# Kernel optimization log

Measured on AMD Instinct MI355X. Metric: run time of the kernel, lower is better.

The kernel has to match this reference:

```python
import jax, jax.numpy as jnp
import numpy as np

N = 100_000      # nodes
DEG = 16         # avg in-degree (fixed per node for setup)
E = N * DEG      # edges
IN = 256         # in_feats
H = 4            # num_heads
D = 64           # out_feats per head
NEG_SLOPE = 0.2


def setup_inputs() -> dict:
    key = jax.random.key(0)
    k1, k2, k3, k4, k5 = jax.random.split(key, 5)
    # dst-major CSR with uniform degree DEG per destination node
    row_ptr = jnp.arange(N + 1, dtype=jnp.int32) * DEG          # [N+1]
    col_ind = jax.random.randint(k1, (E,), 0, N, dtype=jnp.int32)  # source ids per edge
    feat = jax.random.normal(k2, (N, IN), dtype=jnp.float32)
    # fc.weight (xavier-ish scale), torch Linear: y = x @ W.T
    W = jax.random.normal(k3, (H * D, IN), dtype=jnp.float32) * (1.0 / np.sqrt(IN))
    attn_l = jax.random.normal(k4, (1, H, D), dtype=jnp.float32) * 0.1
    attn_r = jax.random.normal(k5, (1, H, D), dtype=jnp.float32) * 0.1
    return {"row_ptr": row_ptr, "col_ind": col_ind, "feat": feat,
            "W": W, "attn_l": attn_l, "attn_r": attn_r}


def reference(row_ptr, col_ind, feat, W, attn_l, attn_r):
    n_nodes = feat.shape[0]
    n_edges = col_ind.shape[0]
    # feat_src = feat_dst = fc(feat).view(-1, H, D)
    feat_src = (feat @ W.T).reshape(n_nodes, H, D)
    el = jnp.sum(feat_src * attn_l, axis=-1)   # [N, H]
    er = jnp.sum(feat_src * attn_r, axis=-1)   # [N, H]
    # per-edge dst id from CSR row_ptr; src = col_ind
    dst = (jnp.searchsorted(row_ptr, jnp.arange(n_edges, dtype=row_ptr.dtype),
                            side='right') - 1).astype(jnp.int32)
    src = col_ind
    # e = u_add_v(g, er, el) -> er[src] + el[dst], then LeakyReLU
    e = er[src] + el[dst]                      # [E, H]
    e = jnp.where(e > 0, e, NEG_SLOPE * e)
    # CSR edge-softmax: normalize over incoming edges of each dst row
    m = jax.ops.segment_max(e, dst, num_segments=n_nodes)    # [N, H]
    ex = jnp.exp(e - m[dst])
    s = jax.ops.segment_sum(ex, dst, num_segments=n_nodes)   # [N, H]
    a = ex / s[dst]                                          # [E, H]
    # multi-head SpMM: out[n,h] = sum_{e: dst=n} a[e,h] * feat_src[src[e],h]
    outs = []
    for h in range(H):  # small fixed head loop to avoid [E,H,D] intermediate
        msg = a[:, h, None] * feat_src[src, h]               # [E, D]
        outs.append(jax.ops.segment_sum(msg, dst, num_segments=n_nodes))
    return jnp.stack(outs, axis=1)                           # [N, H, D]
```

## Files before the change

kernel.cpp:

```cpp
#include <hip/hip_runtime.h>
#include <math.h>


#define HEADS 4
#define KIN 256
#define NOUT 256
#define NEG_SLOPE 0.2f

typedef __attribute__((ext_vector_type(4))) short short4v;
typedef __attribute__((ext_vector_type(8))) short short8v;
typedef __attribute__((ext_vector_type(4))) float floatx4;

static __device__ __forceinline__ unsigned short f2bf(float x) {
  unsigned u = __float_as_uint(x);
  u += 0x7FFFu + ((u >> 16) & 1u);
  return (unsigned short)(u >> 16);
}
static __device__ __forceinline__ float bf2f(unsigned short b) {
  return __uint_as_float(((unsigned)b) << 16);
}

__global__ __launch_bounds__(256) void k_cast_w(const float* __restrict__ W,
                                                unsigned short* __restrict__ Wbf) {
  const int i = blockIdx.x * 256 + threadIdx.x;
  float4 f = ((const float4*)W)[i];
  ushort4 o;
  o.x = f2bf(f.x); o.y = f2bf(f.y); o.z = f2bf(f.z); o.w = f2bf(f.w);
  ((ushort4*)Wbf)[i] = o;
}

__global__ __launch_bounds__(256, 2) void k_gemm_mfma(
    const float* __restrict__ feat, const unsigned short* __restrict__ Wbf,
    const float* __restrict__ attn_l, const float* __restrict__ attn_r,
    unsigned short* __restrict__ fs_bf, float* __restrict__ el,
    float* __restrict__ er, int n_nodes) {
  __shared__ unsigned short Alds[2][64 * 64];

  const int tid = threadIdx.x;
  const int lane = tid & 63;
  const int w = tid >> 6;
  const int m0 = blockIdx.x * 64;
  const int q = lane >> 4;
  const int l15 = lane & 15;

  floatx4 acc[4][4];
#pragma unroll
  for (int mt = 0; mt < 4; ++mt)
#pragma unroll
    for (int nt = 0; nt < 4; ++nt)
#pragma unroll
      for (int r = 0; r < 4; ++r) acc[mt][nt][r] = 0.0f;

  const int ar = tid >> 2;
  const int aj = tid & 3;
  const int r7 = ar & 7;
  int agr = m0 + ar;
  if (agr >= n_nodes) agr = n_nodes - 1;
  const float* __restrict__ abase = feat + (size_t)agr * KIN + aj * 16;
  unsigned short* const aw0 = &Alds[0][ar * 64 + ((2 * aj + 0) ^ r7) * 8];
  unsigned short* const aw1 = &Alds[0][ar * 64 + ((2 * aj + 1) ^ r7) * 8];
  const int bufoff = 64 * 64;

  float4 rg[2][4];

#pragma unroll
  for (int i = 0; i < 4; ++i) rg[0][i] = *(const float4*)(abase + i * 4);

#pragma unroll
  for (int kc = 0; kc < 4; ++kc) {
    const int b = kc & 1;
    {
      const float4* R = rg[b];
      short8v g0, g1;
      g0[0] = (short)f2bf(R[0].x); g0[1] = (short)f2bf(R[0].y);
      g0[2] = (short)f2bf(R[0].z); g0[3] = (short)f2bf(R[0].w);
      g0[4] = (short)f2bf(R[1].x); g0[5] = (short)f2bf(R[1].y);
      g0[6] = (short)f2bf(R[1].z); g0[7] = (short)f2bf(R[1].w);
      g1[0] = (short)f2bf(R[2].x); g1[1] = (short)f2bf(R[2].y);
      g1[2] = (short)f2bf(R[2].z); g1[3] = (short)f2bf(R[2].w);
      g1[4] = (short)f2bf(R[3].x); g1[5] = (short)f2bf(R[3].y);
      g1[6] = (short)f2bf(R[3].z); g1[7] = (short)f2bf(R[3].w);
      *(short8v*)(aw0 + b * bufoff) = g0;
      *(short8v*)(aw1 + b * bufoff) = g1;
    }
    if (kc < 3) {
      const float* p = abase + (kc + 1) * 64;
#pragma unroll
      for (int i = 0; i < 4; ++i) rg[(kc + 1) & 1][i] = *(const float4*)(p + i * 4);
    }
    __syncthreads();

    short8v bfr[2][4];
#pragma unroll
    for (int ks = 0; ks < 2; ++ks)
#pragma unroll
      for (int nt = 0; nt < 4; ++nt)
        bfr[ks][nt] = *(const short8v*)(Wbf + (size_t)(w * 64 + nt * 16 + l15) * KIN +
                                        kc * 64 + ks * 32 + q * 8);

#pragma unroll
    for (int ks = 0; ks < 2; ++ks) {
      short8v af[4];
#pragma unroll
      for (int mt = 0; mt < 4; ++mt) {
        const int slot = (ks * 4 + q) ^ (l15 & 7);
        af[mt] = *(const short8v*)(&Alds[b][(mt * 16 + l15) * 64 + slot * 8]);
      }
#pragma unroll
      for (int mt = 0; mt < 4; ++mt)
#pragma unroll
        for (int nt = 0; nt < 4; ++nt)
          acc[mt][nt] = __builtin_amdgcn_mfma_f32_16x16x32_bf16(
              af[mt], bfr[ks][nt], acc[mt][nt], 0, 0, 0);
    }
  }

  float alv[4], arv[4];
#pragma unroll
  for (int nt = 0; nt < 4; ++nt) {
    alv[nt] = attn_l[w * 64 + nt * 16 + l15];
    arv[nt] = attn_r[w * 64 + nt * 16 + l15];
  }
#pragma unroll
  for (int mt = 0; mt < 4; ++mt) {
#pragma unroll
    for (int r = 0; r < 4; ++r) {
      const int m = m0 + mt * 16 + q * 4 + r;
      const bool mvalid = (m < n_nodes);
      float pl = 0.f, pr = 0.f;
#pragma unroll
      for (int nt = 0; nt < 4; ++nt) {
        const float v = acc[mt][nt][r];
        pl = fmaf(v, alv[nt], pl);
        pr = fmaf(v, arv[nt], pr);
        if (mvalid)
          fs_bf[(size_t)m * NOUT + w * 64 + nt * 16 + l15] = f2bf(v);
      }
#pragma unroll
      for (int off = 1; off < 16; off <<= 1) {
        pl += __shfl_xor(pl, off, 64);
        pr += __shfl_xor(pr, off, 64);
      }
      if (l15 == 0 && mvalid) {
        el[m * HEADS + w] = pl;
        er[m * HEADS + w] = pr;
      }
    }
  }
}

__global__ __launch_bounds__(256, 4) void k_aggregate(
    const int* __restrict__ row_ptr, const int* __restrict__ col_ind,
    const float* __restrict__ el, const float* __restrict__ er,
    const unsigned short* __restrict__ fs_bf, float* __restrict__ out,
    int n_nodes) {
  const int gid = blockIdx.x * blockDim.x + threadIdx.x;
  const int node = gid >> 6;
  const int lane = threadIdx.x & 63;
  if (node >= n_nodes) return;

  const int h = lane >> 4;
  const int j = lane & 15;
  const int rs = row_ptr[node];
  const int deg = row_ptr[node + 1] - rs;

  const bool valid = (j < deg);
  const int src = valid ? col_ind[rs + j] : 0;

  float e = valid ? (er[src * HEADS + h] + el[node * HEADS + h]) : -INFINITY;
  e = (e > 0.f) ? e : NEG_SLOPE * e;

  float mx = e;
#pragma unroll
  for (int off = 1; off < 16; off <<= 1) mx = fmaxf(mx, __shfl_xor(mx, off, 64));
  float ex = valid ? __expf(e - mx) : 0.f;
  float s = ex;
#pragma unroll
  for (int off = 1; off < 16; off <<= 1) s += __shfl_xor(s, off, 64);
  const float a = ex / s;

  const int half = lane >> 5;
  const int li = lane & 31;
  const int hd = li >> 3;

  int sj[8];
#pragma unroll
  for (int p = 0; p < 8; ++p) sj[p] = __shfl(src, 2 * p + half, 64);

  uint4 u[8];
#pragma unroll
  for (int p = 0; p < 8; ++p)
    u[p] = ((const uint4*)(fs_bf + (size_t)sj[p] * NOUT))[li];

  float wgt[8];
#pragma unroll
  for (int p = 0; p < 8; ++p)
    wgt[p] = __shfl(a, hd * 16 + 2 * p + half, 64);

  float acc[8];
#pragma unroll
  for (int k = 0; k < 8; ++k) acc[k] = 0.f;
#pragma unroll
  for (int p = 0; p < 8; ++p) {
    const uint4 v = u[p];
    const float w0 = wgt[p];
    acc[0] = fmaf(w0, __uint_as_float(v.x << 16), acc[0]);
    acc[1] = fmaf(w0, __uint_as_float(v.x & 0xFFFF0000u), acc[1]);
    acc[2] = fmaf(w0, __uint_as_float(v.y << 16), acc[2]);
    acc[3] = fmaf(w0, __uint_as_float(v.y & 0xFFFF0000u), acc[3]);
    acc[4] = fmaf(w0, __uint_as_float(v.z << 16), acc[4]);
    acc[5] = fmaf(w0, __uint_as_float(v.z & 0xFFFF0000u), acc[5]);
    acc[6] = fmaf(w0, __uint_as_float(v.w << 16), acc[6]);
    acc[7] = fmaf(w0, __uint_as_float(v.w & 0xFFFF0000u), acc[7]);
  }

#pragma unroll
  for (int k = 0; k < 8; ++k) acc[k] += __shfl_xor(acc[k], 32, 64);

  float4 o;
  o.x = half ? acc[4] : acc[0];
  o.y = half ? acc[5] : acc[1];
  o.z = half ? acc[6] : acc[2];
  o.w = half ? acc[7] : acc[3];
  *(float4*)(out + (size_t)node * NOUT + li * 8 + half * 4) = o;
}

extern "C" void kernel_launch(void* const* d_in, const int* in_sizes, int n_in,
                              void* d_out, int out_size, void* d_ws, size_t ws_size,
                              hipStream_t stream) {
  const int* row_ptr = (const int*)d_in[0];
  const int* col_ind = (const int*)d_in[1];
  const float* feat = (const float*)d_in[2];
  const float* W = (const float*)d_in[3];
  const float* attn_l = (const float*)d_in[4];
  const float* attn_r = (const float*)d_in[5];
  float* out = (float*)d_out;
  const int n_nodes = in_sizes[0] - 1;

  char* ws = (char*)d_ws;
  unsigned short* Wbf = (unsigned short*)ws;
  unsigned short* fs_bf = (unsigned short*)(ws + 128 * 1024);
  size_t fs_bytes = (size_t)n_nodes * NOUT * sizeof(unsigned short);
  float* el = (float*)(ws + 128 * 1024 + fs_bytes);
  float* er = el + (size_t)n_nodes * HEADS;

  k_cast_w<<<64, 256, 0, stream>>>(W, Wbf);
  k_gemm_mfma<<<(n_nodes + 63) / 64, 256, 0, stream>>>(
      feat, Wbf, attn_l, attn_r, fs_bf, el, er, n_nodes);
  k_aggregate<<<(n_nodes + 3) / 4, 256, 0, stream>>>(
      row_ptr, col_ind, el, er, fs_bf, out, n_nodes);
}
```

Measured before the change: 349.0 us.

## Store projected features head-major and split aggregation per head

Measured after the change: 380.5 us. 9.0% more time.

```diff
diff --git a/kernel.cpp b/kernel.cpp
--- a/kernel.cpp
+++ b/kernel.cpp
@@ -32,8 +32,8 @@
 __global__ __launch_bounds__(256, 2) void k_gemm_mfma(
     const float* __restrict__ feat, const unsigned short* __restrict__ Wbf,
     const float* __restrict__ attn_l, const float* __restrict__ attn_r,
-    unsigned short* __restrict__ fs_bf, float* __restrict__ el,
-    float* __restrict__ er, int n_nodes) {
+    unsigned short* __restrict__ fs_h, float* __restrict__ el_h,
+    float* __restrict__ er_h, int n_nodes) {
   __shared__ unsigned short Alds[2][64 * 64];
 
   const int tid = threadIdx.x;
@@ -134,7 +134,7 @@
         pl = fmaf(v, alv[nt], pl);
         pr = fmaf(v, arv[nt], pr);
         if (mvalid)
-          fs_bf[(size_t)m * NOUT + w * 64 + nt * 16 + l15] = f2bf(v);
+          fs_h[((size_t)w * n_nodes + m) * 64 + nt * 16 + l15] = f2bf(v);
       }
 #pragma unroll
       for (int off = 1; off < 16; off <<= 1) {
@@ -142,8 +142,8 @@
         pr += __shfl_xor(pr, off, 64);
       }
       if (l15 == 0 && mvalid) {
-        el[m * HEADS + w] = pl;
-        er[m * HEADS + w] = pr;
+        el_h[(size_t)w * n_nodes + m] = pl;
+        er_h[(size_t)w * n_nodes + m] = pr;
       }
     }
   }
@@ -151,23 +151,26 @@
 
 __global__ __launch_bounds__(256, 4) void k_aggregate(
     const int* __restrict__ row_ptr, const int* __restrict__ col_ind,
-    const float* __restrict__ el, const float* __restrict__ er,
-    const unsigned short* __restrict__ fs_bf, float* __restrict__ out,
+    const float* __restrict__ el_h, const float* __restrict__ er_h,
+    const unsigned short* __restrict__ fs_h, float* __restrict__ out,
     int n_nodes) {
-  const int gid = blockIdx.x * blockDim.x + threadIdx.x;
-  const int node = gid >> 6;
+  const int bid = blockIdx.x;
   const int lane = threadIdx.x & 63;
+  const int w = threadIdx.x >> 6;
+  const int x = bid & 7;
+  const int h = x >> 1;
+  const int idx = (bid >> 3) * 2 + (x & 1);
+  const int node = idx * 4 + w;
   if (node >= n_nodes) return;
 
-  const int h = lane >> 4;
   const int j = lane & 15;
   const int rs = row_ptr[node];
   const int deg = row_ptr[node + 1] - rs;
-
   const bool valid = (j < deg);
   const int src = valid ? col_ind[rs + j] : 0;
 
-  float e = valid ? (er[src * HEADS + h] + el[node * HEADS + h]) : -INFINITY;
+  const size_t hN = (size_t)h * n_nodes;
+  float e = valid ? (er_h[hN + src] + el_h[hN + node]) : -INFINITY;
   e = (e > 0.f) ? e : NEG_SLOPE * e;
 
   float mx = e;
@@ -179,50 +182,45 @@
   for (int off = 1; off < 16; off <<= 1) s += __shfl_xor(s, off, 64);
   const float a = ex / s;
 
-  const int half = lane >> 5;
-  const int li = lane & 31;
-  const int hd = li >> 3;
-
-  int sj[8];
-#pragma unroll
-  for (int p = 0; p < 8; ++p) sj[p] = __shfl(src, 2 * p + half, 64);
-
-  uint4 u[8];
-#pragma unroll
-  for (int p = 0; p < 8; ++p)
-    u[p] = ((const uint4*)(fs_bf + (size_t)sj[p] * NOUT))[li];
-
-  float wgt[8];
-#pragma unroll
-  for (int p = 0; p < 8; ++p)
-    wgt[p] = __shfl(a, hd * 16 + 2 * p + half, 64);
+  const int e8 = lane >> 3;
+  const int c = lane & 7;
+  const int s0 = __shfl(src, e8, 64);
+  const int s1 = __shfl(src, 8 + e8, 64);
+  const float w0 = __shfl(a, e8, 64);
+  const float w1 = __shfl(a, 8 + e8, 64);
+  const uint4 u0 = ((const uint4*)(fs_h + (hN + (size_t)s0) * 64))[c];
+  const uint4 u1 = ((const uint4*)(fs_h + (hN + (size_t)s1) * 64))[c];
 
   float acc[8];
 #pragma unroll
   for (int k = 0; k < 8; ++k) acc[k] = 0.f;
-#pragma unroll
-  for (int p = 0; p < 8; ++p) {
-    const uint4 v = u[p];
-    const float w0 = wgt[p];
-    acc[0] = fmaf(w0, __uint_as_float(v.x << 16), acc[0]);
-    acc[1] = fmaf(w0, __uint_as_float(v.x & 0xFFFF0000u), acc[1]);
-    acc[2] = fmaf(w0, __uint_as_float(v.y << 16), acc[2]);
-    acc[3] = fmaf(w0, __uint_as_float(v.y & 0xFFFF0000u), acc[3]);
-    acc[4] = fmaf(w0, __uint_as_float(v.z << 16), acc[4]);
-    acc[5] = fmaf(w0, __uint_as_float(v.z & 0xFFFF0000u), acc[5]);
-    acc[6] = fmaf(w0, __uint_as_float(v.w << 16), acc[6]);
-    acc[7] = fmaf(w0, __uint_as_float(v.w & 0xFFFF0000u), acc[7]);
-  }
-
-#pragma unroll
-  for (int k = 0; k < 8; ++k) acc[k] += __shfl_xor(acc[k], 32, 64);
-
-  float4 o;
-  o.x = half ? acc[4] : acc[0];
-  o.y = half ? acc[5] : acc[1];
-  o.z = half ? acc[6] : acc[2];
-  o.w = half ? acc[7] : acc[3];
-  *(float4*)(out + (size_t)node * NOUT + li * 8 + half * 4) = o;
+  acc[0] = fmaf(w0, __uint_as_float(u0.x << 16), acc[0]);
+  acc[1] = fmaf(w0, __uint_as_float(u0.x & 0xFFFF0000u), acc[1]);
+  acc[2] = fmaf(w0, __uint_as_float(u0.y << 16), acc[2]);
+  acc[3] = fmaf(w0, __uint_as_float(u0.y & 0xFFFF0000u), acc[3]);
+  acc[4] = fmaf(w0, __uint_as_float(u0.z << 16), acc[4]);
+  acc[5] = fmaf(w0, __uint_as_float(u0.z & 0xFFFF0000u), acc[5]);
+  acc[6] = fmaf(w0, __uint_as_float(u0.w << 16), acc[6]);
+  acc[7] = fmaf(w0, __uint_as_float(u0.w & 0xFFFF0000u), acc[7]);
+  acc[0] = fmaf(w1, __uint_as_float(u1.x << 16), acc[0]);
+  acc[1] = fmaf(w1, __uint_as_float(u1.x & 0xFFFF0000u), acc[1]);
+  acc[2] = fmaf(w1, __uint_as_float(u1.y << 16), acc[2]);
+  acc[3] = fmaf(w1, __uint_as_float(u1.y & 0xFFFF0000u), acc[3]);
+  acc[4] = fmaf(w1, __uint_as_float(u1.z << 16), acc[4]);
+  acc[5] = fmaf(w1, __uint_as_float(u1.z & 0xFFFF0000u), acc[5]);
+  acc[6] = fmaf(w1, __uint_as_float(u1.w << 16), acc[6]);
+  acc[7] = fmaf(w1, __uint_as_float(u1.w & 0xFFFF0000u), acc[7]);
+
+#pragma unroll
+  for (int off = 8; off < 64; off <<= 1)
+#pragma unroll
+    for (int k = 0; k < 8; ++k) acc[k] += __shfl_xor(acc[k], off, 64);
+
+  if (lane < 8) {
+    float* op = out + ((size_t)node * HEADS + h) * 64 + lane * 8;
+    *(float4*)op = make_float4(acc[0], acc[1], acc[2], acc[3]);
+    *(float4*)(op + 4) = make_float4(acc[4], acc[5], acc[6], acc[7]);
+  }
 }
 
 extern "C" void kernel_launch(void* const* d_in, const int* in_sizes, int n_in,
@@ -239,14 +237,17 @@
 
   char* ws = (char*)d_ws;
   unsigned short* Wbf = (unsigned short*)ws;
-  unsigned short* fs_bf = (unsigned short*)(ws + 128 * 1024);
+  unsigned short* fs_h = (unsigned short*)(ws + 128 * 1024);
   size_t fs_bytes = (size_t)n_nodes * NOUT * sizeof(unsigned short);
-  float* el = (float*)(ws + 128 * 1024 + fs_bytes);
-  float* er = el + (size_t)n_nodes * HEADS;
+  float* el_h = (float*)(ws + 128 * 1024 + fs_bytes);
+  float* er_h = el_h + (size_t)n_nodes * HEADS;
 
   k_cast_w<<<64, 256, 0, stream>>>(W, Wbf);
   k_gemm_mfma<<<(n_nodes + 63) / 64, 256, 0, stream>>>(
-      feat, Wbf, attn_l, attn_r, fs_bf, el, er, n_nodes);
-  k_aggregate<<<(n_nodes + 3) / 4, 256, 0, stream>>>(
-      row_ptr, col_ind, el, er, fs_bf, out, n_nodes);
-}
+      feat, Wbf, attn_l, attn_r, fs_h, el_h, er_h, n_nodes);
+
+  int nb_per_head = (n_nodes + 3) / 4;
+  nb_per_head += (nb_per_head & 1);
+  k_aggregate<<<nb_per_head * 4, 256, 0, stream>>>(
+      row_ptr, col_ind, el_h, er_h, fs_h, out, n_nodes);
+}
```
